# Kernel optimization log

Hardware: AMD Instinct MI355X
Metric: run time of the kernel (lower is better)

Reference implementation:

```python
import jax, jax.numpy as jnp
import numpy as np

A = 8732          # SSD300 anchor count
C = 91            # num classes (incl. background at index 0)
B = 32
IMG = 300.0
SCORE_THRESH = 0.01
NMS_THRESH = 0.45
TOPK = 400        # topk_candidates per class
MAX_DET = 200     # detections_per_img
BBOX_XY_W = 10.0  # box_coder weights (10,10,5,5)
BBOX_WH_W = 5.0
BBOX_CLIP = float(np.log(1000.0 / 16.0))


def setup_inputs() -> dict:
    key = jax.random.key(0)
    k1, k2, kc, ks = jax.random.split(key, 4)
    cls_logits = jax.random.normal(k1, (B, A, C), jnp.float32)
    bbox_regression = jax.random.normal(k2, (B, A, 4), jnp.float32)
    # plausible anchors in xyxy on a 300x300 image
    cxcy = jax.random.uniform(kc, (A, 2), minval=0.0, maxval=IMG)
    wh = jax.random.uniform(ks, (A, 2), minval=10.0, maxval=150.0)
    anchors = jnp.concatenate([cxcy - wh / 2, cxcy + wh / 2], axis=-1)
    return {"cls_logits": cls_logits, "bbox_regression": bbox_regression, "anchors": anchors}


def decode_boxes(rel, anchors):
    wa = anchors[:, 2] - anchors[:, 0]
    ha = anchors[:, 3] - anchors[:, 1]
    cxa = anchors[:, 0] + 0.5 * wa
    cya = anchors[:, 1] + 0.5 * ha
    dx = rel[:, 0] / BBOX_XY_W
    dy = rel[:, 1] / BBOX_XY_W
    dw = jnp.minimum(rel[:, 2] / BBOX_WH_W, BBOX_CLIP)
    dh = jnp.minimum(rel[:, 3] / BBOX_WH_W, BBOX_CLIP)
    cx = dx * wa + cxa
    cy = dy * ha + cya
    w = jnp.exp(dw) * wa
    h = jnp.exp(dh) * ha
    boxes = jnp.stack([cx - 0.5 * w, cy - 0.5 * h, cx + 0.5 * w, cy + 0.5 * h], axis=-1)
    return jnp.clip(boxes, 0.0, IMG)


def iou_one_vs_all(box, boxes):
    # box [4], boxes [N,4] -> [N]
    lt = jnp.maximum(box[:2], boxes[:, :2])
    rb = jnp.minimum(box[2:], boxes[:, 2:])
    wh = jnp.clip(rb - lt, 0.0)
    inter = wh[:, 0] * wh[:, 1]
    a1 = (box[2] - box[0]) * (box[3] - box[1])
    a2 = (boxes[:, 2] - boxes[:, 0]) * (boxes[:, 3] - boxes[:, 1])
    return inter / (a1 + a2 - inter + 1e-9)


def greedy_nms(boxes, scores, iou_thresh, max_det):
    # boxes [N,4] (class-offset), scores [N] (-inf = invalid). Returns top max_det keep idxs.
    def step(sc, _):
        i = jnp.argmax(sc)
        best_sc = sc[i]
        iou = iou_one_vs_all(boxes[i], boxes)
        sc = jnp.where(iou > iou_thresh, -jnp.inf, sc)
        sc = sc.at[i].set(-jnp.inf)
        return sc, (i, best_sc)
    _, (keep, kept_sc) = jax.lax.scan(step, scores, None, length=max_det)
    return keep, kept_sc


def postprocess_one(logits, rel, anchors):
    scores = jax.nn.softmax(logits, axis=-1)      # [A,C]
    boxes = decode_boxes(rel, anchors)            # [A,4]
    fg = scores[:, 1:].T                          # [C-1, A], skip background
    masked = jnp.where(fg > SCORE_THRESH, fg, -jnp.inf)
    top_sc, top_idx = jax.lax.top_k(masked, TOPK)  # [C-1, TOPK]
    cand_boxes = boxes[top_idx].reshape(-1, 4)     # [(C-1)*TOPK, 4]
    cand_sc = top_sc.reshape(-1)
    labels = jnp.broadcast_to(jnp.arange(1, C, dtype=jnp.int32)[:, None], (C - 1, TOPK)).reshape(-1)
    # batched_nms: offset boxes per class so different classes never overlap
    offset = labels.astype(boxes.dtype) * (IMG + 1.0)
    keep, kept_sc = greedy_nms(cand_boxes + offset[:, None], cand_sc, NMS_THRESH, MAX_DET)
    valid = jnp.isfinite(kept_sc)
    out_boxes = jnp.where(valid[:, None], cand_boxes[keep], 0.0)
    out_scores = jnp.where(valid, kept_sc, 0.0)
    out_labels = jnp.where(valid, labels[keep], 0)
    return out_boxes, out_scores, out_labels


def reference(cls_logits, bbox_regression, anchors):
    # returns (boxes [B,200,4], scores [B,200], labels [B,200] int32); invalid slots zeroed
    return jax.vmap(lambda l, r: postprocess_one(l, r, anchors))(cls_logits, bbox_regression)
```

## Files before the change

### kernel.cpp

```cpp
#include <hip/hip_runtime.h>
#include <hip/hip_bf16.h>
#include <cstdint>
#include <cstddef>
#include <math.h>

#pragma clang fp contract(off)

#define A_N 8732
#define C_N 91
#define CM1 90
#define B_N 32
#define TOPK 400
#define MAXDET 200
#define NT 512
#define CCAP 1024
#define BBOX_CLIPF 4.135166556742356f

#define IOU_M ((double)0.45f + 0x1p-26)

typedef float f4u __attribute__((ext_vector_type(4), aligned(4)));

__device__ __forceinline__ float ldin(const void* p, size_t i, int isbf16) {
    if (isbf16) return __bfloat162float(((const __hip_bfloat16*)p)[i]);
    return ((const float*)p)[i];
}

__device__ __forceinline__ float np_expf(float x) {
    float q = rintf(x * 1.442695040f);
    float r = fmaf(q, -0.693359375f, x);
    r = fmaf(q, 2.12194440e-4f, r);
    float p = 1.9875691500E-4f;
    p = fmaf(p, r, 1.3981999507E-3f);
    p = fmaf(p, r, 8.3334519073E-3f);
    p = fmaf(p, r, 4.1665795894E-2f);
    p = fmaf(p, r, 1.6666665459E-1f);
    p = fmaf(p, r, 5.0000001201E-1f);
    p = fmaf(p, r, 1.0f);
    p = fmaf(p, r, 1.0f);
    return ldexpf(p, (int)q);
}

__global__ void k_sniff(const unsigned* __restrict__ words, int* __restrict__ flag) {
    __shared__ int cnt_s;
    if (threadIdx.x == 0) cnt_s = 0;
    __syncthreads();
    int local = 0;
    for (int i = threadIdx.x; i < 4096; i += 256) {
        unsigned w = words[i];
        unsigned e = (w >> 7) & 0xFFu;
        if (e >= 100u && e <= 140u) local++;
    }
    atomicAdd(&cnt_s, local);
    __syncthreads();
    if (threadIdx.x == 0) flag[0] = (cnt_s > 2048) ? 1 : 0;
}

__global__ void k_stats(const void* __restrict__ logits,
                        const void* __restrict__ rel,
                        const void* __restrict__ anchors,
                        const int* __restrict__ flag,
                        float* __restrict__ amax,
                        float* __restrict__ denom,
                        float* __restrict__ boxes,
                        unsigned* __restrict__ scT) {
    int i = blockIdx.x * blockDim.x + threadIdx.x;
    if (i >= B_N * A_N) return;
    int bf = flag[0];
    size_t base = (size_t)i * C_N;
    int bb = i / A_N, aa = i - bb * A_N;
    unsigned* sbase = scT ? (scT + (size_t)bb * CM1 * A_N + aa) : (unsigned*)0;

    if (!bf) {
        const float* lp = (const float*)logits + base;
        float m = -INFINITY;
        #pragma unroll
        for (int k = 0; k < 22; ++k) {
            f4u v = *(const f4u*)(lp + 4 * k);
            m = fmaxf(m, v.x); m = fmaxf(m, v.y); m = fmaxf(m, v.z); m = fmaxf(m, v.w);
        }
        m = fmaxf(m, lp[88]); m = fmaxf(m, lp[89]); m = fmaxf(m, lp[90]);

        float r[8];
        #pragma unroll
        for (int k = 0; k < 11; ++k) {
            f4u v0 = *(const f4u*)(lp + 8 * k);
            f4u v1 = *(const f4u*)(lp + 8 * k + 4);
            float e0 = np_expf(v0.x - m), e1 = np_expf(v0.y - m);
            float e2 = np_expf(v0.z - m), e3 = np_expf(v0.w - m);
            float e4 = np_expf(v1.x - m), e5 = np_expf(v1.y - m);
            float e6 = np_expf(v1.z - m), e7 = np_expf(v1.w - m);
            if (k == 0) {
                r[0] = e0; r[1] = e1; r[2] = e2; r[3] = e3;
                r[4] = e4; r[5] = e5; r[6] = e6; r[7] = e7;
                if (sbase) {
                    sbase[(size_t)0 * A_N] = __float_as_uint(e1);
                    sbase[(size_t)1 * A_N] = __float_as_uint(e2);
                    sbase[(size_t)2 * A_N] = __float_as_uint(e3);
                    sbase[(size_t)3 * A_N] = __float_as_uint(e4);
                    sbase[(size_t)4 * A_N] = __float_as_uint(e5);
                    sbase[(size_t)5 * A_N] = __float_as_uint(e6);
                    sbase[(size_t)6 * A_N] = __float_as_uint(e7);
                }
            } else {
                r[0] += e0; r[1] += e1; r[2] += e2; r[3] += e3;
                r[4] += e4; r[5] += e5; r[6] += e6; r[7] += e7;
                if (sbase) {
                    size_t o = (size_t)(8 * k - 1) * A_N;
                    sbase[o]                  = __float_as_uint(e0);
                    sbase[o + (size_t)1 * A_N] = __float_as_uint(e1);
                    sbase[o + (size_t)2 * A_N] = __float_as_uint(e2);
                    sbase[o + (size_t)3 * A_N] = __float_as_uint(e3);
                    sbase[o + (size_t)4 * A_N] = __float_as_uint(e4);
                    sbase[o + (size_t)5 * A_N] = __float_as_uint(e5);
                    sbase[o + (size_t)6 * A_N] = __float_as_uint(e6);
                    sbase[o + (size_t)7 * A_N] = __float_as_uint(e7);
                }
            }
        }
        float res = ((r[0] + r[1]) + (r[2] + r[3])) + ((r[4] + r[5]) + (r[6] + r[7]));
        float e88 = np_expf(lp[88] - m); res += e88;
        float e89 = np_expf(lp[89] - m); res += e89;
        float e90 = np_expf(lp[90] - m); res += e90;
        if (sbase) {
            sbase[(size_t)87 * A_N] = __float_as_uint(e88);
            sbase[(size_t)88 * A_N] = __float_as_uint(e89);
            sbase[(size_t)89 * A_N] = __float_as_uint(e90);
        }
        amax[i]  = m;
        denom[i] = res;
    } else {
        float m = -INFINITY;
        for (int c = 0; c < C_N; ++c) m = fmaxf(m, ldin(logits, base + c, bf));
        float r[8];
        for (int j = 0; j < 8; ++j) r[j] = np_expf(ldin(logits, base + j, bf) - m);
        for (int c = 8; c < 88; c += 8)
            for (int j = 0; j < 8; ++j) r[j] += np_expf(ldin(logits, base + c + j, bf) - m);
        float res = ((r[0] + r[1]) + (r[2] + r[3])) + ((r[4] + r[5]) + (r[6] + r[7]));
        res += np_expf(ldin(logits, base + 88, bf) - m);
        res += np_expf(ldin(logits, base + 89, bf) - m);
        res += np_expf(ldin(logits, base + 90, bf) - m);
        amax[i]  = m;
        denom[i] = res;
        if (sbase) {
            for (int c = 1; c < C_N; ++c)
                sbase[(size_t)(c - 1) * A_N] =
                    __float_as_uint(np_expf(ldin(logits, base + c, bf) - m));
        }
    }

    {
        int a = aa;
        float ax1, ay1, ax2, ay2, r0, r1, r2, r3;
        if (!bf) {
            float4 av = ((const float4*)anchors)[a];
            float4 rv = ((const float4*)rel)[i];
            ax1 = av.x; ay1 = av.y; ax2 = av.z; ay2 = av.w;
            r0 = rv.x; r1 = rv.y; r2 = rv.z; r3 = rv.w;
        } else {
            ax1 = ldin(anchors, (size_t)a * 4 + 0, bf);
            ay1 = ldin(anchors, (size_t)a * 4 + 1, bf);
            ax2 = ldin(anchors, (size_t)a * 4 + 2, bf);
            ay2 = ldin(anchors, (size_t)a * 4 + 3, bf);
            r0 = ldin(rel, (size_t)i * 4 + 0, bf);
            r1 = ldin(rel, (size_t)i * 4 + 1, bf);
            r2 = ldin(rel, (size_t)i * 4 + 2, bf);
            r3 = ldin(rel, (size_t)i * 4 + 3, bf);
        }
        float wa = ax2 - ax1, ha = ay2 - ay1;
        float cxa = ax1 + 0.5f * wa, cya = ay1 + 0.5f * ha;
        float dx = r0 / 10.0f, dy = r1 / 10.0f;
        float dw = fminf(r2 / 5.0f, BBOX_CLIPF);
        float dh = fminf(r3 / 5.0f, BBOX_CLIPF);
        float cx = dx * wa + cxa, cy = dy * ha + cya;
        float w = np_expf(dw) * wa, h = np_expf(dh) * ha;
        float4 o;
        o.x = fminf(fmaxf(cx - 0.5f * w, 0.0f), 300.0f);
        o.y = fminf(fmaxf(cy - 0.5f * h, 0.0f), 300.0f);
        o.z = fminf(fmaxf(cx + 0.5f * w, 0.0f), 300.0f);
        o.w = fminf(fmaxf(cy + 0.5f * h, 0.0f), 300.0f);
        ((float4*)boxes)[i] = o;
    }
}

__global__ __launch_bounds__(NT) void k_topknms_pre(const unsigned* __restrict__ scT,
                                                    const float* __restrict__ denom,
                                                    const float* __restrict__ boxes,
                                                    unsigned long long* __restrict__ kkey,
                                                    int* __restrict__ kcnt) {
    __shared__ __align__(16) float4 nbq[TOPK];
    __shared__ float sar[TOPK];
    __shared__ unsigned long long wlist[512];
    __shared__ unsigned long long cand[CCAP];
    __shared__ unsigned hist[1024];
    __shared__ unsigned long long fsup[8];
    __shared__ unsigned long long ksv[8];
    __shared__ unsigned sel_b;
    __shared__ int sel_rem;
    __shared__ int nreal_s;
    __shared__ int eqlist[64];
    __shared__ int eqn, nsel, candn, total_s;

    int bc = blockIdx.x;
    int b  = bc / CM1;
    int cm = bc % CM1;
    int t  = threadIdx.x;

    const unsigned* srow = scT + (size_t)bc * A_N;
    const uint4* srow4 = (const uint4*)srow;
    const float4* dnm = (const float4*)(denom + (size_t)b * A_N);
    const float* dsc = denom + (size_t)b * A_N;

    if (t == 0) { eqn = 0; nsel = 0; candn = 0; total_s = 0; }
    for (int q = t; q < 1024; q += NT) hist[q] = 0u;
    __syncthreads();
    for (int k = t; k < A_N / 4; k += NT) {
        uint4 ev = srow4[k];
        float4 dv = dnm[k];
        float s0 = __uint_as_float(ev.x) / dv.x;
        float s1 = __uint_as_float(ev.y) / dv.y;
        float s2 = __uint_as_float(ev.z) / dv.z;
        float s3 = __uint_as_float(ev.w) / dv.w;
        unsigned v0 = (s0 > 0.01f) ? __float_as_uint(s0) : 0u;
        unsigned v1 = (s1 > 0.01f) ? __float_as_uint(s1) : 0u;
        unsigned v2 = (s2 > 0.01f) ? __float_as_uint(s2) : 0u;
        unsigned v3 = (s3 > 0.01f) ? __float_as_uint(s3) : 0u;
        if (v0) atomicAdd(&hist[(v0 >> 16) & 0x3FFu], 1u);
        if (v1) atomicAdd(&hist[(v1 >> 16) & 0x3FFu], 1u);
        if (v2) atomicAdd(&hist[(v2 >> 16) & 0x3FFu], 1u);
        if (v3) atomicAdd(&hist[(v3 >> 16) & 0x3FFu], 1u);
    }
    __syncthreads();

    if (t < 64) {
        unsigned s = 0;
        #pragma unroll
        for (int q = 0; q < 16; ++q) s += hist[16 * t + q];
        unsigned suf = s;
        for (int o = 1; o < 64; o <<= 1) {
            unsigned vv = __shfl_down(suf, o);
            if (t + o < 64) suf += vv;
        }
        if (t == 0) nreal_s = (int)suf;
        unsigned cum = suf - s;
        for (int q = 15; q >= 0; --q) {
            unsigned h = hist[16 * t + q];
            if ((int)cum < TOPK && TOPK <= (int)(cum + h)) {
                sel_b = (unsigned)(16 * t + q);
                sel_rem = TOPK - (int)cum;
            }
            cum += h;
        }
    }
    __syncthreads();
    int nreal = nreal_s;
    bool sel_path = (nreal >= TOPK);
    unsigned selL1 = sel_b;
    unsigned prefix1 = (0xFu << 10) | selL1;
    __syncthreads();

    if (sel_path) { for (int q = t; q < 1024; q += NT) hist[q] = 0u; }
    __syncthreads();
    for (int k = t; k < A_N / 4; k += NT) {
        uint4 ev = srow4[k];
        float4 dv = dnm[k];
        float ss[4];
        ss[0] = __uint_as_float(ev.x) / dv.x;
        ss[1] = __uint_as_float(ev.y) / dv.y;
        ss[2] = __uint_as_float(ev.z) / dv.z;
        ss[3] = __uint_as_float(ev.w) / dv.w;
        #pragma unroll
        for (int c = 0; c < 4; ++c) {
            unsigned v = (ss[c] > 0.01f) ? __float_as_uint(ss[c]) : 0u;
            if (!v) continue;
            unsigned a = (unsigned)(4 * k + c);
            if (sel_path) {
                unsigned bkt = (v >> 16) & 0x3FFu;
                if (bkt > selL1) {
                    int slot = atomicAdd(&nsel, 1);
                    if (slot < 512)
                        wlist[slot] = ((unsigned long long)v << 32) | (unsigned)(~a);
                } else if (bkt == selL1) {
                    int s2 = atomicAdd(&candn, 1);
                    if (s2 < CCAP)
                        cand[s2] = ((unsigned long long)v << 32) | (unsigned)(~a);
                    atomicAdd(&hist[(v >> 6) & 0x3FFu], 1u);
                }
            } else {
                int slot = atomicAdd(&nsel, 1);
                if (slot < 512)
                    wlist[slot] = ((unsigned long long)v << 32) | (unsigned)(~a);
            }
        }
    }
    __syncthreads();

    unsigned sstar = 0u;
    int teq = 0;
    if (sel_path) {
        bool ovf = (candn > CCAP);
        if (t < 64) {
            int rem = sel_rem;
            unsigned s = 0;
            #pragma unroll
            for (int q = 0; q < 16; ++q) s += hist[16 * t + q];
            unsigned suf = s;
            for (int o = 1; o < 64; o <<= 1) {
                unsigned vv = __shfl_down(suf, o);
                if (t + o < 64) suf += vv;
            }
            unsigned cum = suf - s;
            for (int q = 15; q >= 0; --q) {
                unsigned h = hist[16 * t + q];
                if ((int)cum < rem && rem <= (int)(cum + h)) {
                    sel_b = (unsigned)(16 * t + q);
                    sel_rem = rem - (int)cum;
                }
                cum += h;
            }
        }
        __syncthreads();
        unsigned prefix2 = (prefix1 << 10) | sel_b;

        if (t < 64) hist[t] = 0u;
        __syncthreads();
        if (!ovf) {
            int cn = candn < CCAP ? candn : CCAP;
            for (int q = t; q < cn; q += NT) {
                unsigned v = (unsigned)(cand[q] >> 32);
                if ((v >> 6) == prefix2) atomicAdd(&hist[v & 0x3Fu], 1u);
            }
        } else {
            for (int a = t; a < A_N; a += NT) {
                float s = __uint_as_float(srow[a]) / dsc[a];
                unsigned v = (s > 0.01f) ? __float_as_uint(s) : 0u;
                if (v && (v >> 6) == prefix2) atomicAdd(&hist[v & 0x3Fu], 1u);
            }
        }
        __syncthreads();
        if (t == 0) {
            int rem = sel_rem;
            unsigned cum = 0;
            for (int bq = 63; bq >= 0; --bq) {
                unsigned h = hist[bq];
                if ((int)cum < rem && rem <= (int)(cum + h)) {
                    sel_b = (unsigned)bq;
                    sel_rem = rem - (int)cum;
                    break;
                }
                cum += h;
            }
        }
        __syncthreads();
        sstar = (prefix2 << 6) | sel_b;
        teq = sel_rem;

        if (!ovf) {
            int cn = candn < CCAP ? candn : CCAP;
            for (int q = t; q < cn; q += NT) {
                unsigned long long cv = cand[q];
                unsigned v = (unsigned)(cv >> 32);
                if (v > sstar) {
                    int slot = atomicAdd(&nsel, 1);
                    if (slot < 512) wlist[slot] = cv;
                } else if (v == sstar) {
                    int s2 = atomicAdd(&eqn, 1);
                    if (s2 < 64) eqlist[s2] = (int)(~(unsigned)cv);
                }
            }
        } else {
            for (int a = t; a < A_N; a += NT) {
                float s = __uint_as_float(srow[a]) / dsc[a];
                unsigned v = (s > 0.01f) ? __float_as_uint(s) : 0u;
                if (!v) continue;
                if ((v >> 16) == prefix1) {
                    if (v > sstar) {
                        int slot = atomicAdd(&nsel, 1);
                        if (slot < 512)
                            wlist[slot] = ((unsigned long long)v << 32) |
                                          (unsigned)(~(unsigned)a);
                    } else if (v == sstar) {
                        int s2 = atomicAdd(&eqn, 1);
                        if (s2 < 64) eqlist[s2] = a;
                    }
                }
            }
        }
        __syncthreads();
        if (t == 0) {
            int n = eqn < 64 ? eqn : 64;
            for (int i2 = 1; i2 < n; ++i2) {
                int v2 = eqlist[i2], j2 = i2 - 1;
                while (j2 >= 0 && eqlist[j2] > v2) { eqlist[j2 + 1] = eqlist[j2]; --j2; }
                eqlist[j2 + 1] = v2;
            }
            int tq = teq < n ? teq : n;
            int bse = nsel;
            for (int q2 = 0; q2 < tq; ++q2) {
                int slot = bse + q2;
                if (slot < 512)
                    wlist[slot] = ((unsigned long long)sstar << 32) |
                                  (unsigned)(~(unsigned)eqlist[q2]);
            }
            nsel = bse + tq;
        }
        __syncthreads();
    }
    int ns = nsel < 512 ? nsel : 512;
    if (t >= ns) wlist[t] = 0ull;
    __syncthreads();

    {
        unsigned long long u = wlist[t];
        for (int k = 2; k <= 512; k <<= 1) {
            bool up = ((t & k) == 0);
            for (int j = k >> 1; j >= 64; j >>= 1) {
                __syncthreads();
                wlist[t] = u;
                __syncthreads();
                unsigned long long v = wlist[t ^ j];
                bool takeMax = (((t & j) == 0) == up);
                u = takeMax ? (u > v ? u : v) : (u < v ? u : v);
            }
            for (int j = ((k >> 1) < 64 ? (k >> 1) : 32); j > 0; j >>= 1) {
                unsigned long long v = __shfl_xor(u, j);
                bool takeMax = (((t & j) == 0) == up);
                u = takeMax ? (u > v ? u : v) : (u < v ? u : v);
            }
        }
        __syncthreads();
        wlist[t] = u;
        __syncthreads();
    }

    int m = ns < TOPK ? ns : TOPK;
    float offc = (float)(cm + 1) * 301.0f;
    if (t < m) {
        unsigned aidx = ~(unsigned)(wlist[t] & 0xFFFFFFFFull);
        const float* bp = boxes + ((size_t)b * A_N + aidx) * 4;
        float4 q;
        q.x = bp[0] + offc; q.y = bp[1] + offc;
        q.z = bp[2] + offc; q.w = bp[3] + offc;
        nbq[t] = q;
        sar[t] = (q.z - q.x) * (q.w - q.y);
    }
    if (t < 8) { fsup[t] = 0ull; ksv[t] = 0ull; }
    __syncthreads();

    int nch = (m + 63) >> 6;
    for (int g = 0; g < nch; ++g) {
        if (t < 64) {
            int bse = 64 * g;
            int jmax = m - bse; if (jmax > 64) jmax = 64;
            bool valid = t < jmax;
            float4 cb = valid ? nbq[bse + t] : make_float4(0.f, 0.f, 0.f, 0.f);
            float car = valid ? sar[bse + t] : 0.0f;
            unsigned long long sup = fsup[g], kv = 0ull;
            unsigned long long rem =
                ((jmax == 64) ? ~0ull : ((1ull << jmax) - 1ull)) & ~sup;
            while (rem) {
                int j = __builtin_ctzll(rem);
                float rx1 = __shfl(cb.x, j), ry1 = __shfl(cb.y, j);
                float rx2 = __shfl(cb.z, j), ry2 = __shfl(cb.w, j);
                float ra  = __shfl(car, j);
                bool p = false;
                if (valid && t > j) {
                    float lx = fmaxf(rx1, cb.x), ly = fmaxf(ry1, cb.y);
                    float rx = fminf(rx2, cb.z), ry = fminf(ry2, cb.w);
                    float ww = fmaxf(rx - lx, 0.0f), hh = fmaxf(ry - ly, 0.0f);
                    float inter = ww * hh;
                    float U = ra + car - inter + 1e-9f;
                    p = ((double)inter > IOU_M * (double)U);
                }
                unsigned long long wj = __ballot(p);
                kv |= 1ull << j;
                sup |= wj;
                rem &= ~(sup | (1ull << j));
            }
            if (t == 0) { ksv[g] = kv; total_s += __popcll(kv); }
        }
        __syncthreads();
        if (total_s >= MAXDET) break;
        if (g + 1 < nch) {
            int w = t >> 6, l = t & 63;
            int h = g + 1 + w;
            if (h < nch) {
                unsigned long long kv = ksv[g];
                int jmax2 = m - 64 * h; if (jmax2 > 64) jmax2 = 64;
                bool v2 = l < jmax2;
                float4 cbl = v2 ? nbq[64 * h + l] : make_float4(0.f, 0.f, 0.f, 0.f);
                float cal = v2 ? sar[64 * h + l] : 0.0f;
                bool acc = false;
                unsigned long long rr = kv;
                while (rr) {
                    int r = __builtin_ctzll(rr); rr &= rr - 1;
                    float4 rq = nbq[64 * g + r];
                    float rar = sar[64 * g + r];
                    if (v2 && !acc) {
                        float lx = fmaxf(rq.x, cbl.x), ly = fmaxf(rq.y, cbl.y);
                        float rx = fminf(rq.z, cbl.z), ry = fminf(rq.w, cbl.w);
                        float ww = fmaxf(rx - lx, 0.0f), hh = fmaxf(ry - ly, 0.0f);
                        float inter = ww * hh;
                        float U = rar + cal - inter + 1e-9f;
                        acc = ((double)inter > IOU_M * (double)U);
                    }
                }
                unsigned long long wd = __ballot(acc);
                if (l == 0) fsup[h] |= wd;
            }
        }
        __syncthreads();
    }

    if (t < 64) {
        int l = t, basek = 0;
        for (int g = 0; g < nch; ++g) {
            unsigned long long kv = ksv[g];
            int row = 64 * g + l;
            if ((kv >> l) & 1ull) {
                int rank = basek + __popcll(kv & ((1ull << l) - 1ull));
                if (rank < MAXDET) {
                    unsigned long long wv = wlist[row];
                    unsigned sbts = (unsigned)(wv >> 32);
                    unsigned aa2  = ~(unsigned)wv;
                    int flat = cm * TOPK + row;
                    unsigned long long key =
                        ((unsigned long long)sbts << 31) |
                        ((unsigned long long)(131071 - flat) << 14) |
                        (unsigned long long)aa2;
                    kkey[(size_t)bc * MAXDET + rank] = key;
                }
            }
            basek += __popcll(kv);
        }
        if (l == 0) kcnt[bc] = total_s < MAXDET ? total_s : MAXDET;
    }
}

__global__ __launch_bounds__(NT) void k_topknms(const void* __restrict__ logits,
                                                const int* __restrict__ flag,
                                                const float* __restrict__ amax,
                                                const float* __restrict__ denom,
                                                const float* __restrict__ boxes,
                                                unsigned long long* __restrict__ kkey,
                                                int* __restrict__ kcnt) {
    __shared__ union {
        unsigned sbits[A_N];
        unsigned long long msk[TOPK * 7];
    } su;
    __shared__ unsigned long long wlist[512];
    __shared__ float bx1[TOPK], by1[TOPK], bx2[TOPK], by2[TOPK], bar[TOPK];
    __shared__ int wred[NT / 64];
    __shared__ unsigned bcast_p;
    __shared__ int bcast_rem;
    __shared__ int eqlist[64];
    __shared__ int eqn;
    __shared__ int bcast_athr;
    __shared__ int nsel;

    int bc = blockIdx.x;
    int b  = bc / CM1;
    int cm = bc % CM1;
    int bf = flag[0];
    int t  = threadIdx.x;

    for (int a = t; a < A_N; a += NT) {
        size_t base = (size_t)b * A_N + a;
        float e  = np_expf(ldin(logits, base * C_N + (cm + 1), bf) - amax[base]);
        float sc = e / denom[base];
        su.sbits[a] = (sc > 0.01f) ? __float_as_uint(sc) : 0u;
    }
    if (t == 0) { eqn = 0; nsel = 0; }
    __syncthreads();

    {
        int c0 = 0;
        for (int a = t; a < A_N; a += NT) c0 += (su.sbits[a] != 0u);
        for (int o = 32; o; o >>= 1) c0 += __shfl_down(c0, o);
        if ((t & 63) == 0) wred[t >> 6] = c0;
        __syncthreads();
        if (t == 0) {
            int tot = 0;
            for (int wv = 0; wv < NT / 64; ++wv) tot += wred[wv];
            bcast_rem = tot;
        }
        __syncthreads();
    }
    int nreal = bcast_rem;
    __syncthreads();

    unsigned sstar = 0u;
    int teq = 0;
    if (nreal >= TOPK) {
        unsigned p = 0x3C000000u;
        int rem = TOPK;
        for (int bit = 25; bit >= 0; --bit) {
            unsigned q = p | (1u << bit);
            int cnt = 0;
            for (int a = t; a < A_N; a += NT) cnt += ((su.sbits[a] >> bit) == (q >> bit));
            for (int o = 32; o; o >>= 1) cnt += __shfl_down(cnt, o);
            if ((t & 63) == 0) wred[t >> 6] = cnt;
            __syncthreads();
            if (t == 0) {
                int tot = 0;
                for (int wv = 0; wv < NT / 64; ++wv) tot += wred[wv];
                if (tot >= rem) { bcast_p = q; bcast_rem = rem; }
                else            { bcast_p = p; bcast_rem = rem - tot; }
            }
            __syncthreads();
            p = bcast_p; rem = bcast_rem;
            __syncthreads();
        }
        sstar = p;
        teq = rem;
        for (int a = t; a < A_N; a += NT) {
            if (su.sbits[a] == sstar) {
                int slot = atomicAdd(&eqn, 1);
                if (slot < 64) eqlist[slot] = a;
            }
        }
        __syncthreads();
        if (t == 0) {
            int n = eqn < 64 ? eqn : 64;
            for (int i = 1; i < n; ++i) {
                int v = eqlist[i], j = i - 1;
                while (j >= 0 && eqlist[j] > v) { eqlist[j + 1] = eqlist[j]; --j; }
                eqlist[j + 1] = v;
            }
            int tq = teq < n ? teq : n;
            bcast_athr = (tq > 0) ? eqlist[tq - 1] : -1;
        }
        __syncthreads();
    }
    int athr = (nreal >= TOPK) ? bcast_athr : -1;
    __syncthreads();

    for (int a = t; a < A_N; a += NT) {
        unsigned v = su.sbits[a];
        bool sel;
        if (nreal >= TOPK)
            sel = (v > sstar) || (v == sstar && a <= athr);
        else
            sel = (v != 0u);
        if (sel) {
            int slot = atomicAdd(&nsel, 1);
            if (slot < 512)
                wlist[slot] = ((unsigned long long)v << 32) | (unsigned)(~(unsigned)a);
        }
    }
    __syncthreads();
    int ns = nsel < 512 ? nsel : 512;
    if (t < 512 && t >= ns) wlist[t] = 0ull;
    __syncthreads();

    for (int k = 2; k <= 512; k <<= 1) {
        for (int j = k >> 1; j > 0; j >>= 1) {
            int ixj = t ^ j;
            if (ixj > t) {
                unsigned long long u = wlist[t], v = wlist[ixj];
                bool desc = ((t & k) == 0);
                if (desc ? (u < v) : (u > v)) { wlist[t] = v; wlist[ixj] = u; }
            }
            __syncthreads();
        }
    }

    int m = ns < TOPK ? ns : TOPK;
    float offc = (float)(cm + 1) * 301.0f;
    if (t < m) {
        unsigned aidx = ~(unsigned)(wlist[t] & 0xFFFFFFFFull);
        const float* bp = boxes + ((size_t)b * A_N + aidx) * 4;
        float x1 = bp[0] + offc, y1 = bp[1] + offc;
        float x2 = bp[2] + offc, y2 = bp[3] + offc;
        bx1[t] = x1; by1[t] = y1; bx2[t] = x2; by2[t] = y2;
        bar[t] = (x2 - x1) * (y2 - y1);
    }
    __syncthreads();

    if (t < m) {
        unsigned long long w[7] = {0, 0, 0, 0, 0, 0, 0};
        float x1 = bx1[t], y1 = by1[t], x2 = bx2[t], y2 = by2[t], a1 = bar[t];
        for (int j = t + 1; j < m; ++j) {
            float lx = fmaxf(x1, bx1[j]), ly = fmaxf(y1, by1[j]);
            float rx = fminf(x2, bx2[j]), ry = fminf(y2, by2[j]);
            float ww = fmaxf(rx - lx, 0.0f), hh = fmaxf(ry - ly, 0.0f);
            float inter = ww * hh;
            float iou = inter / (a1 + bar[j] - inter + 1e-9f);
            if (iou > 0.45f) w[j >> 6] |= 1ull << (j & 63);
        }
        for (int k2 = 0; k2 < 7; ++k2) su.msk[t * 7 + k2] = w[k2];
    }
    __syncthreads();

    if (t == 0) {
        unsigned long long sup[7] = {0, 0, 0, 0, 0, 0, 0};
        int cnt = 0;
        for (int i = 0; i < m; ++i) {
            if (!((sup[i >> 6] >> (i & 63)) & 1ull)) {
                unsigned long long wv = wlist[i];
                unsigned sb2 = (unsigned)(wv >> 32);
                unsigned a  = ~(unsigned)wv;
                int flat = cm * TOPK + i;
                unsigned long long key =
                    ((unsigned long long)sb2 << 31) |
                    ((unsigned long long)(131071 - flat) << 14) |
                    (unsigned long long)a;
                kkey[(size_t)bc * MAXDET + cnt] = key;
                cnt++;
                if (cnt == MAXDET) break;
                const unsigned long long* r = &su.msk[i * 7];
                for (int k2 = 0; k2 < 7; ++k2) sup[k2] |= r[k2];
            }
        }
        kcnt[bc] = cnt;
    }
}

__global__ __launch_bounds__(256) void k_merge(const unsigned long long* __restrict__ kkey,
                                               const int* __restrict__ kcnt,
                                               const float* __restrict__ boxes,
                                               float* __restrict__ out) {
    __shared__ unsigned hist[1024];
    __shared__ unsigned long long wl[256];
    __shared__ int kc[CM1];
    __shared__ int tot_s;
    __shared__ unsigned selb_s;
    __shared__ int selrem_s;
    __shared__ int gcnt;

    int b = blockIdx.x;
    int t = threadIdx.x;
    const unsigned long long* keys = kkey + (size_t)b * (CM1 * MAXDET);
    const float* bx = boxes + (size_t)b * A_N * 4;
    float* ob = out + (size_t)b * MAXDET * 4;
    float* os = out + (size_t)B_N * MAXDET * 4 + (size_t)b * MAXDET;
    float* ol = out + (size_t)B_N * MAXDET * 5 + (size_t)b * MAXDET;

    if (t < CM1) kc[t] = kcnt[b * CM1 + t];
    if (t == 0) { tot_s = 0; gcnt = 0; }
    __syncthreads();

    {
        int c0 = 0;
        for (int idx = t; idx < CM1 * MAXDET; idx += 256) {
            int c = idx / MAXDET;
            if (idx - c * MAXDET < kc[c]) c0++;
        }
        for (int o = 32; o; o >>= 1) c0 += __shfl_down(c0, o);
        if ((t & 63) == 0) atomicAdd(&tot_s, c0);
    }
    __syncthreads();
    int total = tot_s;

    unsigned long long T = 0ull;
    if (total > MAXDET) {
        unsigned long long prefix = 0ull;
        if (t == 0) selrem_s = MAXDET;
        __syncthreads();
        const int sh[7] = {52, 42, 32, 22, 12, 2, 0};
        const int wd[7] = {10, 10, 10, 10, 10, 10, 2};
        for (int l = 0; l < 7; ++l) {
            int shift = sh[l], width = wd[l];
            int nb = 1 << width;
            for (int q = t; q < nb; q += 256) hist[q] = 0u;
            __syncthreads();
            for (int idx = t; idx < CM1 * MAXDET; idx += 256) {
                int c = idx / MAXDET;
                if (idx - c * MAXDET < kc[c]) {
                    unsigned long long key = keys[idx];
                    if ((key >> (shift + width)) == prefix)
                        atomicAdd(&hist[(unsigned)(key >> shift) & (unsigned)(nb - 1)], 1u);
                }
            }
            __syncthreads();
            if (nb >= 64) {
                if (t < 64) {
                    int rem = selrem_s;
                    int per = nb / 64;
                    unsigned s = 0;
                    for (int q = 0; q < per; ++q) s += hist[per * t + q];
                    unsigned suf = s;
                    for (int o = 1; o < 64; o <<= 1) {
                        unsigned vv = __shfl_down(suf, o);
                        if (t + o < 64) suf += vv;
                    }
                    unsigned cum = suf - s;
                    for (int q = per - 1; q >= 0; --q) {
                        unsigned h = hist[per * t + q];
                        if ((int)cum < rem && rem <= (int)(cum + h)) {
                            selb_s = (unsigned)(per * t + q);
                            selrem_s = rem - (int)cum;
                        }
                        cum += h;
                    }
                }
            } else if (t == 0) {
                int rem = selrem_s;
                unsigned cum = 0;
                for (int bq = nb - 1; bq >= 0; --bq) {
                    unsigned h = hist[bq];
                    if ((int)cum < rem && rem <= (int)(cum + h)) {
                        selb_s = (unsigned)bq;
                        selrem_s = rem - (int)cum;
                        break;
                    }
                    cum += h;
                }
            }
            __syncthreads();
            prefix = (prefix << width) | (unsigned long long)selb_s;
            __syncthreads();
        }
        T = prefix;
    }

    wl[t] = 0ull;
    __syncthreads();
    for (int idx = t; idx < CM1 * MAXDET; idx += 256) {
        int c = idx / MAXDET;
        if (idx - c * MAXDET < kc[c]) {
            unsigned long long key = keys[idx];
            if (key >= T) {
                int s = atomicAdd(&gcnt, 1);
                if (s < 256) wl[s] = key;
            }
        }
    }
    __syncthreads();

    for (int k = 2; k <= 256; k <<= 1) {
        for (int j = k >> 1; j > 0; j >>= 1) {
            int ixj = t ^ j;
            if (ixj > t) {
                unsigned long long u = wl[t], v = wl[ixj];
                bool desc = ((t & k) == 0);
                if (desc ? (u < v) : (u > v)) { wl[t] = v; wl[ixj] = u; }
            }
            __syncthreads();
        }
    }

    if (t < MAXDET) {
        unsigned long long key = wl[t];
        if (key == 0ull) {
            ob[t * 4 + 0] = 0.0f; ob[t * 4 + 1] = 0.0f;
            ob[t * 4 + 2] = 0.0f; ob[t * 4 + 3] = 0.0f;
            os[t] = 0.0f; ol[t] = 0.0f;
        } else {
            int a = (int)(key & 0x3FFFull);
            int flat = 131071 - (int)((key >> 14) & 0x1FFFFull);
            int cmv = flat / TOPK;
            const float* bp = bx + (size_t)a * 4;
            ob[t * 4 + 0] = bp[0]; ob[t * 4 + 1] = bp[1];
            ob[t * 4 + 2] = bp[2]; ob[t * 4 + 3] = bp[3];
            os[t] = __uint_as_float((unsigned)(key >> 31));
            ol[t] = (float)(cmv + 1);
        }
    }
}

extern "C" void kernel_launch(void* const* d_in, const int* in_sizes, int n_in,
                              void* d_out, int out_size, void* d_ws, size_t ws_size,
                              hipStream_t stream) {
    const void* logits  = d_in[0];
    const void* rel     = d_in[1];
    const void* anchors = d_in[2];
    float* out = (float*)d_out;

    char* ws = (char*)d_ws;
    size_t off = 0;
    auto alloc = [&](size_t bytes) -> void* {
        void* p = ws + off;
        off = (off + bytes + 255) & ~(size_t)255;
        return p;
    };
    float* boxes  = (float*)alloc((size_t)B_N * A_N * 4 * sizeof(float));
    float* amax   = (float*)alloc((size_t)B_N * A_N * sizeof(float));
    float* denom  = (float*)alloc((size_t)B_N * A_N * sizeof(float));
    int*   flag   = (int*)alloc(256);
    unsigned long long* kkey = (unsigned long long*)alloc((size_t)B_N * CM1 * MAXDET * sizeof(unsigned long long));
    int* kcnt     = (int*)alloc((size_t)B_N * CM1 * sizeof(int));

    size_t scT_bytes = (size_t)B_N * CM1 * A_N * sizeof(unsigned);
    unsigned* scT = nullptr;
    if (off + scT_bytes <= ws_size) scT = (unsigned*)alloc(scT_bytes);

    int gridBA = (B_N * A_N + 255) / 256;

    k_sniff<<<1, 256, 0, stream>>>((const unsigned*)logits, flag);
    k_stats<<<gridBA, 256, 0, stream>>>(logits, rel, anchors, flag, amax, denom, boxes, scT);
    if (scT)
        k_topknms_pre<<<B_N * CM1, NT, 0, stream>>>(scT, denom, boxes, kkey, kcnt);
    else
        k_topknms<<<B_N * CM1, NT, 0, stream>>>(logits, flag, amax, denom, boxes, kkey, kcnt);
    k_merge<<<B_N, 256, 0, stream>>>(kkey, kcnt, boxes, out);
}
```

Baseline: 652.6 us.

## Precompute thresholded softmax scores in stats kernel and shortcut top-k selection

```diff
diff --git a/kernel.cpp b/kernel.cpp
--- a/kernel.cpp
+++ b/kernel.cpp
@@ -72,62 +72,43 @@
 
     if (!bf) {
         const float* lp = (const float*)logits + base;
-        float m = -INFINITY;
+        float x[91];
         #pragma unroll
         for (int k = 0; k < 22; ++k) {
             f4u v = *(const f4u*)(lp + 4 * k);
-            m = fmaxf(m, v.x); m = fmaxf(m, v.y); m = fmaxf(m, v.z); m = fmaxf(m, v.w);
-        }
-        m = fmaxf(m, lp[88]); m = fmaxf(m, lp[89]); m = fmaxf(m, lp[90]);
+            x[4 * k + 0] = v.x; x[4 * k + 1] = v.y;
+            x[4 * k + 2] = v.z; x[4 * k + 3] = v.w;
+        }
+        x[88] = lp[88]; x[89] = lp[89]; x[90] = lp[90];
+
+        float m = -INFINITY;
+        #pragma unroll
+        for (int c = 0; c < 91; ++c) m = fmaxf(m, x[c]);
+
+        #pragma unroll
+        for (int c = 0; c < 91; ++c) x[c] = np_expf(x[c] - m);
 
         float r[8];
         #pragma unroll
-        for (int k = 0; k < 11; ++k) {
-            f4u v0 = *(const f4u*)(lp + 8 * k);
-            f4u v1 = *(const f4u*)(lp + 8 * k + 4);
-            float e0 = np_expf(v0.x - m), e1 = np_expf(v0.y - m);
-            float e2 = np_expf(v0.z - m), e3 = np_expf(v0.w - m);
-            float e4 = np_expf(v1.x - m), e5 = np_expf(v1.y - m);
-            float e6 = np_expf(v1.z - m), e7 = np_expf(v1.w - m);
-            if (k == 0) {
-                r[0] = e0; r[1] = e1; r[2] = e2; r[3] = e3;
-                r[4] = e4; r[5] = e5; r[6] = e6; r[7] = e7;
-                if (sbase) {
-                    sbase[(size_t)0 * A_N] = __float_as_uint(e1);
-                    sbase[(size_t)1 * A_N] = __float_as_uint(e2);
-                    sbase[(size_t)2 * A_N] = __float_as_uint(e3);
-                    sbase[(size_t)3 * A_N] = __float_as_uint(e4);
-                    sbase[(size_t)4 * A_N] = __float_as_uint(e5);
-                    sbase[(size_t)5 * A_N] = __float_as_uint(e6);
-                    sbase[(size_t)6 * A_N] = __float_as_uint(e7);
-                }
-            } else {
-                r[0] += e0; r[1] += e1; r[2] += e2; r[3] += e3;
-                r[4] += e4; r[5] += e5; r[6] += e6; r[7] += e7;
-                if (sbase) {
-                    size_t o = (size_t)(8 * k - 1) * A_N;
-                    sbase[o]                  = __float_as_uint(e0);
-                    sbase[o + (size_t)1 * A_N] = __float_as_uint(e1);
-                    sbase[o + (size_t)2 * A_N] = __float_as_uint(e2);
-                    sbase[o + (size_t)3 * A_N] = __float_as_uint(e3);
-                    sbase[o + (size_t)4 * A_N] = __float_as_uint(e4);
-                    sbase[o + (size_t)5 * A_N] = __float_as_uint(e5);
-                    sbase[o + (size_t)6 * A_N] = __float_as_uint(e6);
-                    sbase[o + (size_t)7 * A_N] = __float_as_uint(e7);
-                }
-            }
+        for (int j = 0; j < 8; ++j) {
+            float s = x[j];
+            #pragma unroll
+            for (int k = 1; k < 11; ++k) s += x[8 * k + j];
+            r[j] = s;
         }
         float res = ((r[0] + r[1]) + (r[2] + r[3])) + ((r[4] + r[5]) + (r[6] + r[7]));
-        float e88 = np_expf(lp[88] - m); res += e88;
-        float e89 = np_expf(lp[89] - m); res += e89;
-        float e90 = np_expf(lp[90] - m); res += e90;
-        if (sbase) {
-            sbase[(size_t)87 * A_N] = __float_as_uint(e88);
-            sbase[(size_t)88 * A_N] = __float_as_uint(e89);
-            sbase[(size_t)89 * A_N] = __float_as_uint(e90);
-        }
+        res += x[88]; res += x[89]; res += x[90];
         amax[i]  = m;
         denom[i] = res;
+
+        if (sbase) {
+            #pragma unroll
+            for (int c = 1; c < 91; ++c) {
+                float sc = x[c] / res;
+                sbase[(size_t)(c - 1) * A_N] =
+                    (sc > 0.01f) ? __float_as_uint(sc) : 0u;
+            }
+        }
     } else {
         float m = -INFINITY;
         for (int c = 0; c < C_N; ++c) m = fmaxf(m, ldin(logits, base + c, bf));
@@ -142,9 +123,11 @@
         amax[i]  = m;
         denom[i] = res;
         if (sbase) {
-            for (int c = 1; c < C_N; ++c)
+            for (int c = 1; c < C_N; ++c) {
+                float sc = np_expf(ldin(logits, base + c, bf) - m) / res;
                 sbase[(size_t)(c - 1) * A_N] =
-                    __float_as_uint(np_expf(ldin(logits, base + c, bf) - m));
+                    (sc > 0.01f) ? __float_as_uint(sc) : 0u;
+            }
         }
     }
 
@@ -183,7 +166,6 @@
 }
 
 __global__ __launch_bounds__(NT) void k_topknms_pre(const unsigned* __restrict__ scT,
-                                                    const float* __restrict__ denom,
                                                     const float* __restrict__ boxes,
                                                     unsigned long long* __restrict__ kkey,
                                                     int* __restrict__ kcnt) {
@@ -207,27 +189,16 @@
 
     const unsigned* srow = scT + (size_t)bc * A_N;
     const uint4* srow4 = (const uint4*)srow;
-    const float4* dnm = (const float4*)(denom + (size_t)b * A_N);
-    const float* dsc = denom + (size_t)b * A_N;
 
     if (t == 0) { eqn = 0; nsel = 0; candn = 0; total_s = 0; }
     for (int q = t; q < 1024; q += NT) hist[q] = 0u;
     __syncthreads();
     for (int k = t; k < A_N / 4; k += NT) {
-        uint4 ev = srow4[k];
-        float4 dv = dnm[k];
-        float s0 = __uint_as_float(ev.x) / dv.x;
-        float s1 = __uint_as_float(ev.y) / dv.y;
-        float s2 = __uint_as_float(ev.z) / dv.z;
-        float s3 = __uint_as_float(ev.w) / dv.w;
-        unsigned v0 = (s0 > 0.01f) ? __float_as_uint(s0) : 0u;
-        unsigned v1 = (s1 > 0.01f) ? __float_as_uint(s1) : 0u;
-        unsigned v2 = (s2 > 0.01f) ? __float_as_uint(s2) : 0u;
-        unsigned v3 = (s3 > 0.01f) ? __float_as_uint(s3) : 0u;
-        if (v0) atomicAdd(&hist[(v0 >> 16) & 0x3FFu], 1u);
-        if (v1) atomicAdd(&hist[(v1 >> 16) & 0x3FFu], 1u);
-        if (v2) atomicAdd(&hist[(v2 >> 16) & 0x3FFu], 1u);
-        if (v3) atomicAdd(&hist[(v3 >> 16) & 0x3FFu], 1u);
+        uint4 v = srow4[k];
+        if (v.x) atomicAdd(&hist[(v.x >> 16) & 0x3FFu], 1u);
+        if (v.y) atomicAdd(&hist[(v.y >> 16) & 0x3FFu], 1u);
+        if (v.z) atomicAdd(&hist[(v.z >> 16) & 0x3FFu], 1u);
+        if (v.w) atomicAdd(&hist[(v.w >> 16) & 0x3FFu], 1u);
     }
     __syncthreads();
 
@@ -261,16 +232,11 @@
     if (sel_path) { for (int q = t; q < 1024; q += NT) hist[q] = 0u; }
     __syncthreads();
     for (int k = t; k < A_N / 4; k += NT) {
-        uint4 ev = srow4[k];
-        float4 dv = dnm[k];
-        float ss[4];
-        ss[0] = __uint_as_float(ev.x) / dv.x;
-        ss[1] = __uint_as_float(ev.y) / dv.y;
-        ss[2] = __uint_as_float(ev.z) / dv.z;
-        ss[3] = __uint_as_float(ev.w) / dv.w;
+        uint4 vv = srow4[k];
+        unsigned va[4] = {vv.x, vv.y, vv.z, vv.w};
         #pragma unroll
         for (int c = 0; c < 4; ++c) {
-            unsigned v = (ss[c] > 0.01f) ? __float_as_uint(ss[c]) : 0u;
+            unsigned v = va[c];
             if (!v) continue;
             unsigned a = (unsigned)(4 * k + c);
             if (sel_path) {
@@ -294,116 +260,122 @@
     }
     __syncthreads();
 
-    unsigned sstar = 0u;
-    int teq = 0;
     if (sel_path) {
-        bool ovf = (candn > CCAP);
-        if (t < 64) {
-            int rem = sel_rem;
-            unsigned s = 0;
-            #pragma unroll
-            for (int q = 0; q < 16; ++q) s += hist[16 * t + q];
-            unsigned suf = s;
-            for (int o = 1; o < 64; o <<= 1) {
-                unsigned vv = __shfl_down(suf, o);
-                if (t + o < 64) suf += vv;
-            }
-            unsigned cum = suf - s;
-            for (int q = 15; q >= 0; --q) {
-                unsigned h = hist[16 * t + q];
-                if ((int)cum < rem && rem <= (int)(cum + h)) {
-                    sel_b = (unsigned)(16 * t + q);
-                    sel_rem = rem - (int)cum;
-                }
-                cum += h;
-            }
-        }
-        __syncthreads();
-        unsigned prefix2 = (prefix1 << 10) | sel_b;
-
-        if (t < 64) hist[t] = 0u;
-        __syncthreads();
-        if (!ovf) {
-            int cn = candn < CCAP ? candn : CCAP;
-            for (int q = t; q < cn; q += NT) {
-                unsigned v = (unsigned)(cand[q] >> 32);
-                if ((v >> 6) == prefix2) atomicAdd(&hist[v & 0x3Fu], 1u);
-            }
+        int ngt = nsel;
+        int cn  = candn;
+        bool fast = (cn <= CCAP) && (ngt + cn <= 512);
+        if (fast) {
+            for (int q = t; q < cn; q += NT) wlist[ngt + q] = cand[q];
+            __syncthreads();
+            if (t == 0) nsel = ngt + cn;
+            __syncthreads();
         } else {
-            for (int a = t; a < A_N; a += NT) {
-                float s = __uint_as_float(srow[a]) / dsc[a];
-                unsigned v = (s > 0.01f) ? __float_as_uint(s) : 0u;
-                if (v && (v >> 6) == prefix2) atomicAdd(&hist[v & 0x3Fu], 1u);
-            }
-        }
-        __syncthreads();
-        if (t == 0) {
-            int rem = sel_rem;
-            unsigned cum = 0;
-            for (int bq = 63; bq >= 0; --bq) {
-                unsigned h = hist[bq];
-                if ((int)cum < rem && rem <= (int)(cum + h)) {
-                    sel_b = (unsigned)bq;
-                    sel_rem = rem - (int)cum;
-                    break;
-                }
-                cum += h;
-            }
-        }
-        __syncthreads();
-        sstar = (prefix2 << 6) | sel_b;
-        teq = sel_rem;
-
-        if (!ovf) {
-            int cn = candn < CCAP ? candn : CCAP;
-            for (int q = t; q < cn; q += NT) {
-                unsigned long long cv = cand[q];
-                unsigned v = (unsigned)(cv >> 32);
-                if (v > sstar) {
-                    int slot = atomicAdd(&nsel, 1);
-                    if (slot < 512) wlist[slot] = cv;
-                } else if (v == sstar) {
-                    int s2 = atomicAdd(&eqn, 1);
-                    if (s2 < 64) eqlist[s2] = (int)(~(unsigned)cv);
-                }
-            }
-        } else {
-            for (int a = t; a < A_N; a += NT) {
-                float s = __uint_as_float(srow[a]) / dsc[a];
-                unsigned v = (s > 0.01f) ? __float_as_uint(s) : 0u;
-                if (!v) continue;
-                if ((v >> 16) == prefix1) {
+            bool ovf = (cn > CCAP);
+            if (t < 64) {
+                int rem = sel_rem;
+                unsigned s = 0;
+                #pragma unroll
+                for (int q = 0; q < 16; ++q) s += hist[16 * t + q];
+                unsigned suf = s;
+                for (int o = 1; o < 64; o <<= 1) {
+                    unsigned vv = __shfl_down(suf, o);
+                    if (t + o < 64) suf += vv;
+                }
+                unsigned cum = suf - s;
+                for (int q = 15; q >= 0; --q) {
+                    unsigned h = hist[16 * t + q];
+                    if ((int)cum < rem && rem <= (int)(cum + h)) {
+                        sel_b = (unsigned)(16 * t + q);
+                        sel_rem = rem - (int)cum;
+                    }
+                    cum += h;
+                }
+            }
+            __syncthreads();
+            unsigned prefix2 = (prefix1 << 10) | sel_b;
+
+            if (t < 64) hist[t] = 0u;
+            __syncthreads();
+            if (!ovf) {
+                int cc = cn < CCAP ? cn : CCAP;
+                for (int q = t; q < cc; q += NT) {
+                    unsigned v = (unsigned)(cand[q] >> 32);
+                    if ((v >> 6) == prefix2) atomicAdd(&hist[v & 0x3Fu], 1u);
+                }
+            } else {
+                for (int a = t; a < A_N; a += NT) {
+                    unsigned v = srow[a];
+                    if (v && (v >> 6) == prefix2) atomicAdd(&hist[v & 0x3Fu], 1u);
+                }
+            }
+            __syncthreads();
+            if (t == 0) {
+                int rem = sel_rem;
+                unsigned cum = 0;
+                for (int bq = 63; bq >= 0; --bq) {
+                    unsigned h = hist[bq];
+                    if ((int)cum < rem && rem <= (int)(cum + h)) {
+                        sel_b = (unsigned)bq;
+                        sel_rem = rem - (int)cum;
+                        break;
+                    }
+                    cum += h;
+                }
+            }
+            __syncthreads();
+            unsigned sstar = (prefix2 << 6) | sel_b;
+            int teq = sel_rem;
+
+            if (!ovf) {
+                int cc = cn < CCAP ? cn : CCAP;
+                for (int q = t; q < cc; q += NT) {
+                    unsigned long long cv = cand[q];
+                    unsigned v = (unsigned)(cv >> 32);
                     if (v > sstar) {
                         int slot = atomicAdd(&nsel, 1);
-                        if (slot < 512)
-                            wlist[slot] = ((unsigned long long)v << 32) |
-                                          (unsigned)(~(unsigned)a);
+                        if (slot < 512) wlist[slot] = cv;
                     } else if (v == sstar) {
                         int s2 = atomicAdd(&eqn, 1);
-                        if (s2 < 64) eqlist[s2] = a;
+                        if (s2 < 64) eqlist[s2] = (int)(~(unsigned)cv);
                     }
                 }
-            }
-        }
-        __syncthreads();
-        if (t == 0) {
-            int n = eqn < 64 ? eqn : 64;
-            for (int i2 = 1; i2 < n; ++i2) {
-                int v2 = eqlist[i2], j2 = i2 - 1;
-                while (j2 >= 0 && eqlist[j2] > v2) { eqlist[j2 + 1] = eqlist[j2]; --j2; }
-                eqlist[j2 + 1] = v2;
-            }
-            int tq = teq < n ? teq : n;
-            int bse = nsel;
-            for (int q2 = 0; q2 < tq; ++q2) {
-                int slot = bse + q2;
-                if (slot < 512)
-                    wlist[slot] = ((unsigned long long)sstar << 32) |
-                                  (unsigned)(~(unsigned)eqlist[q2]);
-            }
-            nsel = bse + tq;
-        }
-        __syncthreads();
+            } else {
+                for (int a = t; a < A_N; a += NT) {
+                    unsigned v = srow[a];
+                    if (!v) continue;
+                    if ((v >> 16) == prefix1) {
+                        if (v > sstar) {
+                            int slot = atomicAdd(&nsel, 1);
+                            if (slot < 512)
+                                wlist[slot] = ((unsigned long long)v << 32) |
+                                              (unsigned)(~(unsigned)a);
+                        } else if (v == sstar) {
+                            int s2 = atomicAdd(&eqn, 1);
+                            if (s2 < 64) eqlist[s2] = a;
+                        }
+                    }
+                }
+            }
+            __syncthreads();
+            if (t == 0) {
+                int n = eqn < 64 ? eqn : 64;
+                for (int i2 = 1; i2 < n; ++i2) {
+                    int v2 = eqlist[i2], j2 = i2 - 1;
+                    while (j2 >= 0 && eqlist[j2] > v2) { eqlist[j2 + 1] = eqlist[j2]; --j2; }
+                    eqlist[j2 + 1] = v2;
+                }
+                int tq = teq < n ? teq : n;
+                int bse = nsel;
+                for (int q2 = 0; q2 < tq; ++q2) {
+                    int slot = bse + q2;
+                    if (slot < 512)
+                        wlist[slot] = ((unsigned long long)sstar << 32) |
+                                      (unsigned)(~(unsigned)eqlist[q2]);
+                }
+                nsel = bse + tq;
+            }
+            __syncthreads();
+        }
     }
     int ns = nsel < 512 ? nsel : 512;
     if (t >= ns) wlist[t] = 0ull;
@@ -454,11 +426,8 @@
             bool valid = t < jmax;
             float4 cb = valid ? nbq[bse + t] : make_float4(0.f, 0.f, 0.f, 0.f);
             float car = valid ? sar[bse + t] : 0.0f;
-            unsigned long long sup = fsup[g], kv = 0ull;
-            unsigned long long rem =
-                ((jmax == 64) ? ~0ull : ((1ull << jmax) - 1ull)) & ~sup;
-            while (rem) {
-                int j = __builtin_ctzll(rem);
+            unsigned long long w = 0ull;
+            for (int j = 0; j < jmax; ++j) {
                 float rx1 = __shfl(cb.x, j), ry1 = __shfl(cb.y, j);
                 float rx2 = __shfl(cb.z, j), ry2 = __shfl(cb.w, j);
                 float ra  = __shfl(car, j);
@@ -471,7 +440,15 @@
                     float U = ra + car - inter + 1e-9f;
                     p = ((double)inter > IOU_M * (double)U);
                 }
-                unsigned long long wj = __ballot(p);
+                unsigned long long bj = __ballot(p);
+                if (t == j) w = bj;
+            }
+            unsigned long long sup = fsup[g], kv = 0ull;
+            unsigned long long rem =
+                ((jmax == 64) ? ~0ull : ((1ull << jmax) - 1ull)) & ~sup;
+            while (rem) {
+                int j = __builtin_ctzll(rem);
+                unsigned long long wj = __shfl(w, j);
                 kv |= 1ull << j;
                 sup |= wj;
                 rem &= ~(sup | (1ull << j));
@@ -889,7 +866,7 @@
     k_sniff<<<1, 256, 0, stream>>>((const unsigned*)logits, flag);
     k_stats<<<gridBA, 256, 0, stream>>>(logits, rel, anchors, flag, amax, denom, boxes, scT);
     if (scT)
-        k_topknms_pre<<<B_N * CM1, NT, 0, stream>>>(scT, denom, boxes, kkey, kcnt);
+        k_topknms_pre<<<B_N * CM1, NT, 0, stream>>>(scT, boxes, kkey, kcnt);
     else
         k_topknms<<<B_N * CM1, NT, 0, stream>>>(logits, flag, amax, denom, boxes, kkey, kcnt);
     k_merge<<<B_N, 256, 0, stream>>>(kkey, kcnt, boxes, out);
```

After: 736.9 us. 12.9% more time.
